# Optimization experiments

Measured on AMD Instinct MI355X. Metric: run time of the kernel, lower is better.

Reference implementation:

```python
import jax, jax.numpy as jnp
import numpy as np

B, F, Hh, Ww, C = 1, 8, 12, 18, 1920
HEADS, HD, RANK, TXT = 30, 64, 128, 224
VID = F * Hh * Ww  # 1728
DN = ('NCH', 'OIH', 'NCH')


def setup_inputs() -> dict:
    key = jax.random.key(0)
    ks = jax.random.split(key, 14)
    s = 0.02
    return {
        'hidden_states': jax.random.normal(ks[0], (B, VID, C), jnp.float32),
        'encoder_hidden_states': jax.random.normal(ks[1], (B, TXT, C), jnp.float32),
        'cos': jax.random.uniform(ks[2], (VID, HD), jnp.float32),
        'sin': jax.random.uniform(ks[3], (VID, HD), jnp.float32),
        'conv1_w': jax.random.normal(ks[4], (RANK, C, 3), jnp.float32) * s,
        'conv2_w': jax.random.normal(ks[5], (C, RANK, 3), jnp.float32) * s,
        'Wq': jax.random.normal(ks[6], (C, C), jnp.float32) * s,
        'bq': jnp.zeros((C,), jnp.float32),
        'Wk': jax.random.normal(ks[7], (C, C), jnp.float32) * s,
        'bk': jnp.zeros((C,), jnp.float32),
        'Wv': jax.random.normal(ks[8], (C, C), jnp.float32) * s,
        'bv': jnp.zeros((C,), jnp.float32),
        'Wo': jax.random.normal(ks[9], (C, C), jnp.float32) * s,
        'bo': jnp.zeros((C,), jnp.float32),
    }


def _rope(x, cos, sin):
    # x: [B, H, S_vid, D]; cos/sin: [S_vid, D]; interleaved rotate-half
    xr = x.reshape(*x.shape[:-1], -1, 2)
    x_rot = jnp.stack([-xr[..., 1], xr[..., 0]], axis=-1).reshape(x.shape)
    return x * cos + x_rot * sin


def reference(hidden_states, encoder_hidden_states, cos, sin, conv1_w, conv2_w,
              Wq, bq, Wk, bk, Wv, bv, Wo, bo):
    # temporal conv1d skip branch over frame axis per spatial location
    x = hidden_states.reshape(B, F, Hh, Ww, C).transpose(0, 2, 3, 4, 1)
    x = x.reshape(B * Hh * Ww, C, F)
    h = jax.lax.conv_general_dilated(x, conv1_w, (1,), [(1, 1)], dimension_numbers=DN)
    h = jax.nn.gelu(h, approximate=False)
    h = jax.lax.conv_general_dilated(h, conv2_w, (1,), [(1, 1)], dimension_numbers=DN)
    skip = h.reshape(B, Hh, Ww, C, F).transpose(0, 4, 1, 2, 3).reshape(B, VID, C)

    hs = jnp.concatenate([encoder_hidden_states, hidden_states + skip], axis=1)  # [B,S,C]

    q = (hs @ Wq.T + bq).reshape(B, -1, HEADS, HD).transpose(0, 2, 1, 3)
    k = (hs @ Wk.T + bk).reshape(B, -1, HEADS, HD).transpose(0, 2, 1, 3)
    v = (hs @ Wv.T + bv).reshape(B, -1, HEADS, HD).transpose(0, 2, 1, 3)

    # RoPE applied only to the video (image) tokens of q and k
    q = jnp.concatenate([q[:, :, :TXT], _rope(q[:, :, TXT:], cos, sin)], axis=2)
    k = jnp.concatenate([k[:, :, :TXT], _rope(k[:, :, TXT:], cos, sin)], axis=2)

    scores = jnp.einsum('bhqd,bhkd->bhqk', q, k) * (HD ** -0.5)
    attn = jax.nn.softmax(scores, axis=-1)
    o = jnp.einsum('bhqk,bhkd->bhqd', attn, v)
    o = o.transpose(0, 2, 1, 3).reshape(B, -1, HEADS * HD)
    o = o @ Wo.T + bo  # to_out[0]; to_out[1] is dropout (identity at eval)

    return (o[:, TXT:], o[:, :TXT])  # (hidden_states, encoder_hidden_states)
```

## Files before the change

kernel.cpp:

```cpp
#include <hip/hip_runtime.h>
#include <math.h>

typedef unsigned short u16;
typedef short short8 __attribute__((ext_vector_type(8)));
typedef short shortv4 __attribute__((ext_vector_type(4)));
typedef float f32x4 __attribute__((ext_vector_type(4)));

#define TXT 224
#define VID 1728
#define S_ALL 1952
#define C_DIM 1920
#define HD 64
#define RANK 128
#define SHD 124928

#define OFF_HS   ((size_t)0)
#define OFF_XPAD ((size_t)3932160)
#define OFF_O    OFF_XPAD
#define OFF_HG   ((size_t)8355840)
#define OFF_W1T  ((size_t)8650752)
#define OFF_W2T  ((size_t)9388032)
#define OFF_WQ   ((size_t)10125312)
#define OFF_WK   ((size_t)13811712)
#define OFF_WV   ((size_t)17498112)
#define OFF_WO   ((size_t)21184512)
#define OFF_Q    ((size_t)24870912)
#define OFF_K    ((size_t)28618752)
#define OFF_V    ((size_t)32366592)

__device__ __forceinline__ float b2f(u16 u) {
  union { unsigned int i; float f; } x; x.i = ((unsigned int)u) << 16; return x.f;
}
__device__ __forceinline__ u16 f2b(float f) {
  union { float f; unsigned int i; } x; x.f = f;
  unsigned int i = x.i;
  return (u16)((i + 0x7FFFu + ((i >> 16) & 1u)) >> 16);
}
__device__ __forceinline__ void gload16(const u16* g, short* l) {
  __builtin_amdgcn_global_load_lds((const __attribute__((address_space(1))) unsigned int*)g,
                                   (__attribute__((address_space(3))) unsigned int*)l, 16, 0, 0);
}

__global__ void __launch_bounds__(256) prep_kernel(const float* __restrict__ hidden,
                                                   const float* __restrict__ enc,
                                                   const float* __restrict__ w1,
                                                   const float* __restrict__ w2,
                                                   const float* __restrict__ Wq,
                                                   const float* __restrict__ Wk,
                                                   const float* __restrict__ Wv,
                                                   const float* __restrict__ Wo,
                                                   u16* __restrict__ ws) {
  size_t i = (size_t)blockIdx.x * 256 + threadIdx.x;
  if (i < 1105920) {
    const size_t e = i * 4;
    const int row = (int)(e / 1920), col = (int)(e % 1920);
    shortv4 o4 = {0, 0, 0, 0};
    if (row >= 216 && row < 1944) {
      const float4 f = *(const float4*)(hidden + (size_t)(row - 216) * 1920 + col);
      o4 = (shortv4){(short)f2b(f.x), (short)f2b(f.y), (short)f2b(f.z), (short)f2b(f.w)};
    }
    *(shortv4*)(ws + OFF_XPAD + e) = o4;
    return;
  }
  i -= 1105920;
  if (i < 184320) {
    const size_t e = i * 4;
    const int r = (int)(e / 5760), j = (int)(e % 5760), t = j / 1920, c = j % 1920;
    const float* s = w1 + (size_t)r * 5760 + (size_t)c * 3 + t;
    shortv4 o4 = {(short)f2b(s[0]), (short)f2b(s[3]), (short)f2b(s[6]), (short)f2b(s[9])};
    *(shortv4*)(ws + OFF_W1T + e) = o4;
    return;
  }
  i -= 184320;
  if (i < 184320) {
    const size_t e = i * 4;
    const int c = (int)(e / 384), j = (int)(e % 384), t = j / 128, r = j % 128;
    const float* s = w2 + (size_t)c * 384 + (size_t)r * 3 + t;
    shortv4 o4 = {(short)f2b(s[0]), (short)f2b(s[3]), (short)f2b(s[6]), (short)f2b(s[9])};
    *(shortv4*)(ws + OFF_W2T + e) = o4;
    return;
  }
  i -= 184320;
  if (i < 107520) {
    const size_t e = i * 4;
    const float4 f = *(const float4*)(enc + e);
    *(shortv4*)(ws + OFF_HS + e) =
        (shortv4){(short)f2b(f.x), (short)f2b(f.y), (short)f2b(f.z), (short)f2b(f.w)};
    return;
  }
  i -= 107520;
  if (i < 3686400) {
    const int j = (int)(i / 921600);
    const size_t e = (i - (size_t)j * 921600) * 4;
    const float* src = (j == 0) ? Wq : ((j == 1) ? Wk : ((j == 2) ? Wv : Wo));
    const float4 f = *(const float4*)(src + e);
    *(shortv4*)(ws + OFF_WQ + (size_t)j * 3686400 + e) =
        (shortv4){(short)f2b(f.x), (short)f2b(f.y), (short)f2b(f.z), (short)f2b(f.w)};
    return;
  }
  i -= 3686400;
  const short8 z8 = {0, 0, 0, 0, 0, 0, 0, 0};
  size_t e;
  if (i < 23040) e = OFF_HS + 3747840 + i * 8;
  else if (i < 26496) e = OFF_HG + (i - 23040) * 8;
  else if (i < 32256) e = OFF_HG + 248832 + (i - 26496) * 8;
  else e = OFF_O + 3747840 + (i - 32256) * 8;
  *(short8*)(ws + e) = z8;
}

struct GArgs {
  const u16 *A, *B0, *B1, *B2;
  const float *bias0, *bias1, *bias2;
  const float *cosp, *sinp, *hidden;
  u16 *out0, *out1, *out2;
  float* outf;
  int lda, ldb, ksteps, spt, tap_rows, nMt, nNt, Mvalid;
};

template <int BM, int BN, int EPI>
__global__ void __launch_bounds__(256) gemm_bt(GArgs a) {
  constexpr int WM = BM / 2, WN = BN / 2, FM = WM / 16, FN = WN / 16;
  __shared__ __align__(16) short lA[BM * 32];
  __shared__ __align__(16) short lB[BN * 32];
  const int tid = threadIdx.x;
  const int lane = tid & 63;
  const int wv = tid >> 6, wr = wv >> 1, wc = wv & 1;
  const int lr = lane & 15, lg = lane >> 4;
  const int mtile = blockIdx.x % a.nMt;
  const int ntile_raw = blockIdx.x / a.nMt;
  const int ntile = ntile_raw % a.nNt;
  const int slice = ntile_raw / a.nNt;
  const int kstart = slice * a.ksteps;
  const int sec = (ntile * BN) / C_DIM;
  const u16* Bw = (sec == 0) ? a.B0 : ((sec == 1) ? a.B1 : a.B2);
  const int nb = ntile * BN - sec * C_DIM;
  const int m0 = mtile * BM;

  f32x4 acc[FM][FN];
#pragma unroll
  for (int i = 0; i < FM; ++i)
#pragma unroll
    for (int j = 0; j < FN; ++j) acc[i][j] = (f32x4){0.f, 0.f, 0.f, 0.f};

  for (int s = 0; s < a.ksteps; ++s) {
    const int gs = kstart + s;
    const int tap = gs / a.spt;
    const int kcol = (gs - tap * a.spt) * 32;
    const int arow0 = m0 + tap * a.tap_rows;
#pragma unroll
    for (int i = 0; i < BM / 64; ++i) {
      const int o = (i * 256 + tid) * 16;
      const int row = o >> 6;
      const int ke = (o & 63) >> 1;
      gload16(a.A + (size_t)(arow0 + row) * a.lda + (kcol + ke), lA + (o >> 1));
    }
#pragma unroll
    for (int i = 0; i < BN / 64; ++i) {
      const int o = (i * 256 + tid) * 16;
      const int row = o >> 6;
      const int ke = (o & 63) >> 1;
      gload16(Bw + (size_t)(nb + row) * a.ldb + (gs * 32 + ke), lB + (o >> 1));
    }
    __syncthreads();
    short8 af[FM], bfr[FN];
#pragma unroll
    for (int i = 0; i < FM; ++i)
      af[i] = *(const short8*)(lA + (wr * WM + i * 16 + lr) * 32 + lg * 8);
#pragma unroll
    for (int j = 0; j < FN; ++j)
      bfr[j] = *(const short8*)(lB + (wc * WN + j * 16 + lr) * 32 + lg * 8);
#pragma unroll
    for (int i = 0; i < FM; ++i)
#pragma unroll
      for (int j = 0; j < FN; ++j)
        acc[i][j] = __builtin_amdgcn_mfma_f32_16x16x32_bf16(af[i], bfr[j], acc[i][j], 0, 0, 0);
    __syncthreads();
  }

#pragma unroll
  for (int i = 0; i < FM; ++i) {
#pragma unroll
    for (int j = 0; j < FN; ++j) {
      const int col = ntile * BN + wc * WN + j * 16 + lr;
#pragma unroll
      for (int r = 0; r < 4; ++r) {
        const int m = m0 + wr * WM + i * 16 + lg * 4 + r;
        float v = acc[i][j][r];
        if (EPI == 4) {
          if (m < a.Mvalid) a.outf[(size_t)slice * 221184 + (size_t)m * RANK + col] = v;
        } else if (EPI == 1) {
          if (m < a.Mvalid) {
            v += a.hidden[(size_t)m * C_DIM + col];
            a.out0[(size_t)m * C_DIM + col] = f2b(v);
          }
        } else if (EPI == 2) {
          const int nn = col - sec * C_DIM;
          const int hh = nn >> 6, d = nn & 63;
          const float* bias = (sec == 0) ? a.bias0 : ((sec == 1) ? a.bias1 : a.bias2);
          v += bias[nn];
          const float vp = __shfl_xor(v, 1);
          if (sec < 2 && m >= TXT) {
            const int vid = ((m < S_ALL) ? m : TXT) - TXT;
            const float c = a.cosp[vid * HD + d];
            const float sn = a.sinp[vid * HD + d];
            v = (d & 1) ? (v * c + vp * sn) : (v * c - vp * sn);
          }
          if (sec == 0) v *= 0.18033688011112042f;
          if (m < a.Mvalid) {
            u16* dst = (sec == 0) ? a.out0 : ((sec == 1) ? a.out1 : a.out2);
            dst[(size_t)hh * SHD + (size_t)m * HD + d] = f2b(v);
          }
        } else {
          v += a.bias0[col];
          if (m < a.Mvalid) {
            const int dr = (m >= TXT) ? (m - TXT) : (VID + m);
            a.outf[(size_t)dr * C_DIM + col] = v;
          }
        }
      }
    }
  }
}

__global__ void __launch_bounds__(256) c1reduce_kernel(const float* __restrict__ part,
                                                       u16* __restrict__ hg) {
  const int i = blockIdx.x * 256 + threadIdx.x;
  float s = 0.f;
#pragma unroll
  for (int j = 0; j < 6; ++j) s += part[(size_t)j * 221184 + i];
  const float g = 0.5f * s * (1.0f + erff(s * 0.70710678f));
  hg[i] = f2b(g);
}

__global__ void __launch_bounds__(256) vtrans_kernel(const u16* __restrict__ vin,
                                                     u16* __restrict__ vout) {
  __shared__ u16 t[64][72];
  const int b = blockIdx.x, hh = b / 31, mt = b % 31;
  const int m0 = mt * 64;
  const int rows = (m0 + 64 <= S_ALL) ? 64 : (S_ALL - m0);
  const int tid = threadIdx.x;
  const u16* src = vin + (size_t)hh * SHD + (size_t)m0 * HD;
#pragma unroll
  for (int p = 0; p < 2; ++p) {
    const int r = p * 32 + (tid >> 3), c = (tid & 7) * 8;
    short8 v8 = {0, 0, 0, 0, 0, 0, 0, 0};
    if (r < rows) v8 = *(const short8*)(src + (size_t)r * HD + c);
    *(short8*)&t[r][c] = v8;
  }
  __syncthreads();
  const int d = tid & 63, ms = tid >> 6;
  if (ms * 16 < rows) {
    short8 a0, a1;
#pragma unroll
    for (int x = 0; x < 8; ++x) { a0[x] = (short)t[ms * 16 + x][d]; a1[x] = (short)t[ms * 16 + 8 + x][d]; }
    u16* dst = vout + (size_t)hh * SHD + (size_t)d * S_ALL + m0 + ms * 16;
    *(short8*)dst = a0;
    *(short8*)(dst + 8) = a1;
  }
}

__global__ void __launch_bounds__(256) attn_kernel(const u16* __restrict__ q,
                                                   const u16* __restrict__ k,
                                                   const u16* __restrict__ vT,
                                                   u16* __restrict__ o) {
  __shared__ __align__(16) short lK[2][4096];
  __shared__ __align__(16) short lV[2][4096];
  __shared__ __align__(16) short lp[4][1024];
  const int bid = blockIdx.x;
  const int hh = bid / 31, qt = bid - hh * 31;
  const int tid = threadIdx.x, wv = tid >> 6, lane = tid & 63;
  const int lr = lane & 15, lg = lane >> 4;
  const int qbase = qt * 64 + wv * 16;
  const bool active = qbase < S_ALL;
  const u16* qh = q + (size_t)hh * SHD;
  const u16* kh = k + (size_t)hh * SHD;
  const u16* vh = vT + (size_t)hh * SHD;

  int krow[2], kcol[2], kdst[2];
#pragma unroll
  for (int j = 0; j < 2; ++j) {
    const int p0 = (j * 256 + tid) * 8;
    const int row = p0 >> 6, cs = p0 & 63;
    kdst[j] = p0;
    krow[j] = row;
    kcol[j] = cs ^ ((row & 7) * 8);
  }

  short8 aq0 = {}, aq1 = {};
  if (active) {
    aq0 = *(const short8*)(qh + (size_t)(qbase + lr) * HD + lg * 8);
    aq1 = *(const short8*)(qh + (size_t)(qbase + lr) * HD + 32 + lg * 8);
  }
  f32x4 oa[4];
#pragma unroll
  for (int gd = 0; gd < 4; ++gd) oa[gd] = (f32x4){0.f, 0.f, 0.f, 0.f};
  float mr = -3.0e38f, lw = 0.f;
  const f32x4 z4 = (f32x4){0.f, 0.f, 0.f, 0.f};
  const int pmask = (lr & 7) * 8;
  short* lpw = &lp[wv][0];

#pragma unroll
  for (int j = 0; j < 2; ++j) gload16(kh + (size_t)krow[j] * HD + kcol[j], &lK[0][kdst[j]]);
#pragma unroll
  for (int j = 0; j < 2; ++j) gload16(vh + (size_t)krow[j] * S_ALL + kcol[j], &lV[0][kdst[j]]);
  __syncthreads();

  int cur = 0;
  for (int t = 0; t < 30; ++t) {
    if (t < 29) {
      const int kb = (t + 1) * 64;
#pragma unroll
      for (int j = 0; j < 2; ++j)
        gload16(kh + (size_t)(kb + krow[j]) * HD + kcol[j], &lK[cur ^ 1][kdst[j]]);
#pragma unroll
      for (int j = 0; j < 2; ++j)
        gload16(vh + (size_t)krow[j] * S_ALL + (kb + kcol[j]), &lV[cur ^ 1][kdst[j]]);
    }
    if (active) {
      const short* Kt = &lK[cur][0];
      const short* Vt = &lV[cur][0];
      f32x4 st[4];
      __builtin_amdgcn_s_setprio(1);
#pragma unroll
      for (int k16 = 0; k16 < 4; ++k16) {
        const int row = k16 * 16 + lr;
        const int m8 = (row & 7) * 8;
        short8 kf0 = *(const short8*)(Kt + row * 64 + ((lg * 8) ^ m8));
        short8 kf1 = *(const short8*)(Kt + row * 64 + ((32 + lg * 8) ^ m8));
        st[k16] = __builtin_amdgcn_mfma_f32_16x16x32_bf16(kf0, aq0, z4, 0, 0, 0);
        st[k16] = __builtin_amdgcn_mfma_f32_16x16x32_bf16(kf1, aq1, st[k16], 0, 0, 0);
      }
      __builtin_amdgcn_s_setprio(0);
      float tm = fmaxf(fmaxf(fmaxf(st[0][0], st[0][1]), fmaxf(st[0][2], st[0][3])),
                       fmaxf(fmaxf(st[1][0], st[1][1]), fmaxf(st[1][2], st[1][3])));
      tm = fmaxf(tm, fmaxf(fmaxf(fmaxf(st[2][0], st[2][1]), fmaxf(st[2][2], st[2][3])),
                           fmaxf(fmaxf(st[3][0], st[3][1]), fmaxf(st[3][2], st[3][3]))));
      tm = fmaxf(tm, __shfl_xor(tm, 16));
      tm = fmaxf(tm, __shfl_xor(tm, 32));
      const bool defer = (__all(tm <= mr + 8.0f) != 0);
      float al = 1.0f;
      if (!defer) {
        const float mn = fmaxf(mr, tm);
        al = __builtin_exp2f(mr - mn);
        mr = mn;
      }
      float rs = 0.f;
#pragma unroll
      for (int k16 = 0; k16 < 4; ++k16) {
        float p0 = __builtin_exp2f(st[k16][0] - mr);
        float p1 = __builtin_exp2f(st[k16][1] - mr);
        float p2 = __builtin_exp2f(st[k16][2] - mr);
        float p3 = __builtin_exp2f(st[k16][3] - mr);
        rs += (p0 + p1) + (p2 + p3);
        uint2 pk;
        asm("v_cvt_pk_bf16_f32 %0, %1, %2" : "=v"(pk.x) : "v"(p0), "v"(p1));
        asm("v_cvt_pk_bf16_f32 %0, %1, %2" : "=v"(pk.y) : "v"(p2), "v"(p3));
        *(uint2*)(lpw + lr * 64 + ((k16 * 16 + lg * 4) ^ pmask)) = pk;
      }
      rs += __shfl_xor(rs, 16);
      rs += __shfl_xor(rs, 32);
      lw = lw * al + rs;
      asm volatile("s_waitcnt lgkmcnt(0)" ::: "memory");
      short8 pa0 = *(const short8*)(lpw + lr * 64 + ((lg * 8) ^ pmask));
      short8 pa1 = *(const short8*)(lpw + lr * 64 + ((32 + lg * 8) ^ pmask));
      float alp[4];
      if (!defer) {
#pragma unroll
        for (int r = 0; r < 4; ++r) alp[r] = __shfl(al, lg * 4 + r);
      }
      __builtin_amdgcn_s_setprio(1);
#pragma unroll
      for (int gd = 0; gd < 4; ++gd) {
        const int row = gd * 16 + lr;
        const int m8 = (row & 7) * 8;
        short8 vf0 = *(const short8*)(Vt + row * 64 + ((lg * 8) ^ m8));
        short8 vf1 = *(const short8*)(Vt + row * 64 + ((32 + lg * 8) ^ m8));
        f32x4 tacc = oa[gd];
        if (!defer) {
#pragma unroll
          for (int r = 0; r < 4; ++r) tacc[r] *= alp[r];
        }
        tacc = __builtin_amdgcn_mfma_f32_16x16x32_bf16(pa0, vf0, tacc, 0, 0, 0);
        oa[gd] = __builtin_amdgcn_mfma_f32_16x16x32_bf16(pa1, vf1, tacc, 0, 0, 0);
      }
      __builtin_amdgcn_s_setprio(0);
    }
    __syncthreads();
    cur ^= 1;
  }

  if (active) {
    const u16* kp = kh + (size_t)1920 * HD;
    short8 kf00 = *(const short8*)(kp + (size_t)lr * HD + lg * 8);
    short8 kf01 = *(const short8*)(kp + (size_t)lr * HD + 32 + lg * 8);
    short8 kf10 = *(const short8*)(kp + (size_t)(16 + lr) * HD + lg * 8);
    short8 kf11 = *(const short8*)(kp + (size_t)(16 + lr) * HD + 32 + lg * 8);
    f32x4 st0 = __builtin_amdgcn_mfma_f32_16x16x32_bf16(kf00, aq0, z4, 0, 0, 0);
    st0 = __builtin_amdgcn_mfma_f32_16x16x32_bf16(kf01, aq1, st0, 0, 0, 0);
    f32x4 st1 = __builtin_amdgcn_mfma_f32_16x16x32_bf16(kf10, aq0, z4, 0, 0, 0);
    st1 = __builtin_amdgcn_mfma_f32_16x16x32_bf16(kf11, aq1, st1, 0, 0, 0);
    float tm = fmaxf(fmaxf(fmaxf(st0[0], st0[1]), fmaxf(st0[2], st0[3])),
                     fmaxf(fmaxf(st1[0], st1[1]), fmaxf(st1[2], st1[3])));
    tm = fmaxf(tm, __shfl_xor(tm, 16));
    tm = fmaxf(tm, __shfl_xor(tm, 32));
    const float mn = fmaxf(mr, tm);
    const float al = __builtin_exp2f(mr - mn);
    mr = mn;
    float rs = 0.f;
    float pp[8];
#pragma unroll
    for (int r = 0; r < 4; ++r) { pp[r] = __builtin_exp2f(st0[r] - mn); rs += pp[r]; }
#pragma unroll
    for (int r = 0; r < 4; ++r) { pp[4 + r] = __builtin_exp2f(st1[r] - mn); rs += pp[4 + r]; }
    {
      uint2 pk;
      asm("v_cvt_pk_bf16_f32 %0, %1, %2" : "=v"(pk.x) : "v"(pp[0]), "v"(pp[1]));
      asm("v_cvt_pk_bf16_f32 %0, %1, %2" : "=v"(pk.y) : "v"(pp[2]), "v"(pp[3]));
      *(uint2*)(lpw + lr * 64 + ((lg * 4) ^ pmask)) = pk;
      asm("v_cvt_pk_bf16_f32 %0, %1, %2" : "=v"(pk.x) : "v"(pp[4]), "v"(pp[5]));
      asm("v_cvt_pk_bf16_f32 %0, %1, %2" : "=v"(pk.y) : "v"(pp[6]), "v"(pp[7]));
      *(uint2*)(lpw + lr * 64 + ((16 + lg * 4) ^ pmask)) = pk;
    }
    rs += __shfl_xor(rs, 16);
    rs += __shfl_xor(rs, 32);
    lw = lw * al + rs;
    asm volatile("s_waitcnt lgkmcnt(0)" ::: "memory");
    short8 pa0 = *(const short8*)(lpw + lr * 64 + ((lg * 8) ^ pmask));
    float alp[4];
#pragma unroll
    for (int r = 0; r < 4; ++r) alp[r] = __shfl(al, lg * 4 + r);
#pragma unroll
    for (int gd = 0; gd < 4; ++gd) {
      short8 vf = *(const short8*)(vh + (size_t)(gd * 16 + lr) * S_ALL + 1920 + lg * 8);
      f32x4 tacc = oa[gd];
#pragma unroll
      for (int r = 0; r < 4; ++r) tacc[r] *= alp[r];
      oa[gd] = __builtin_amdgcn_mfma_f32_16x16x32_bf16(pa0, vf, tacc, 0, 0, 0);
    }
    float lwp[4];
#pragma unroll
    for (int r = 0; r < 4; ++r) lwp[r] = 1.0f / __shfl(lw, lg * 4 + r);
#pragma unroll
    for (int gd = 0; gd < 4; ++gd) {
      const int col = hh * HD + gd * 16 + lr;
#pragma unroll
      for (int r = 0; r < 4; ++r) {
        const int m = qbase + lg * 4 + r;
        o[(size_t)m * C_DIM + col] = f2b(oa[gd][r] * lwp[r]);
      }
    }
  }
}

extern "C" void kernel_launch(void* const* d_in, const int* in_sizes, int n_in,
                              void* d_out, int out_size, void* d_ws, size_t ws_size,
                              hipStream_t stream) {
  const float* hidden = (const float*)d_in[0];
  const float* enc = (const float*)d_in[1];
  const float* cosp = (const float*)d_in[2];
  const float* sinp = (const float*)d_in[3];
  const float* w1 = (const float*)d_in[4];
  const float* w2 = (const float*)d_in[5];
  const float* bq = (const float*)d_in[7];
  const float* bk = (const float*)d_in[9];
  const float* bv = (const float*)d_in[11];
  const float* bo = (const float*)d_in[13];
  u16* ws = (u16*)d_ws;
  float* out = (float*)d_out;

  prep_kernel<<<20796, 256, 0, stream>>>(hidden, enc, w1, w2, (const float*)d_in[6],
                                         (const float*)d_in[8], (const float*)d_in[10],
                                         (const float*)d_in[12], ws);

  GArgs c1{};
  c1.A = ws + OFF_XPAD; c1.B0 = c1.B1 = c1.B2 = ws + OFF_W1T;
  c1.lda = C_DIM; c1.ldb = 5760; c1.ksteps = 30; c1.spt = 60; c1.tap_rows = 216;
  c1.nMt = 27; c1.nNt = 2; c1.Mvalid = VID;
  c1.outf = (float*)(ws + OFF_Q);
  gemm_bt<64, 64, 4><<<324, 256, 0, stream>>>(c1);

  c1reduce_kernel<<<864, 256, 0, stream>>>((const float*)(ws + OFF_Q),
                                           ws + OFF_HG + (size_t)216 * RANK);

  GArgs c2{};
  c2.A = ws + OFF_HG; c2.B0 = c2.B1 = c2.B2 = ws + OFF_W2T;
  c2.lda = RANK; c2.ldb = 384; c2.ksteps = 12; c2.spt = 4; c2.tap_rows = 216;
  c2.nMt = 14; c2.nNt = 15; c2.Mvalid = VID; c2.hidden = hidden;
  c2.out0 = ws + OFF_HS + (size_t)TXT * C_DIM;
  gemm_bt<128, 128, 1><<<210, 256, 0, stream>>>(c2);

  GArgs c3{};
  c3.A = ws + OFF_HS; c3.B0 = ws + OFF_WQ; c3.B1 = ws + OFF_WK; c3.B2 = ws + OFF_WV;
  c3.bias0 = bq; c3.bias1 = bk; c3.bias2 = bv; c3.cosp = cosp; c3.sinp = sinp;
  c3.lda = C_DIM; c3.ldb = C_DIM; c3.ksteps = 60; c3.spt = 60; c3.tap_rows = 0;
  c3.nMt = 16; c3.nNt = 45; c3.Mvalid = S_ALL;
  c3.out0 = ws + OFF_Q; c3.out1 = ws + OFF_K; c3.out2 = ws + OFF_O;
  gemm_bt<128, 128, 2><<<720, 256, 0, stream>>>(c3);

  vtrans_kernel<<<930, 256, 0, stream>>>(ws + OFF_O, ws + OFF_V);

  attn_kernel<<<930, 256, 0, stream>>>(ws + OFF_Q, ws + OFF_K, ws + OFF_V, ws + OFF_O);

  GArgs c4{};
  c4.A = ws + OFF_O; c4.B0 = c4.B1 = c4.B2 = ws + OFF_WO; c4.bias0 = bo;
  c4.lda = C_DIM; c4.ldb = C_DIM; c4.ksteps = 60; c4.spt = 60; c4.tap_rows = 0;
  c4.nMt = 32; c4.nNt = 15; c4.Mvalid = S_ALL;
  c4.outf = out;
  gemm_bt<64, 128, 3><<<480, 256, 0, stream>>>(c4);
}
```

Measured before the change: 273.2 us.

## Double-buffer GEMM LDS tiles and load attention K/V directly from global

```diff
diff --git a/kernel.cpp b/kernel.cpp
--- a/kernel.cpp
+++ b/kernel.cpp
@@ -120,8 +120,8 @@
 template <int BM, int BN, int EPI>
 __global__ void __launch_bounds__(256) gemm_bt(GArgs a) {
   constexpr int WM = BM / 2, WN = BN / 2, FM = WM / 16, FN = WN / 16;
-  __shared__ __align__(16) short lA[BM * 32];
-  __shared__ __align__(16) short lB[BN * 32];
+  __shared__ __align__(16) short lA[2][BM * 32];
+  __shared__ __align__(16) short lB[2][BN * 32];
   const int tid = threadIdx.x;
   const int lane = tid & 63;
   const int wv = tid >> 6, wr = wv >> 1, wc = wv & 1;
@@ -142,8 +142,7 @@
 #pragma unroll
     for (int j = 0; j < FN; ++j) acc[i][j] = (f32x4){0.f, 0.f, 0.f, 0.f};
 
-  for (int s = 0; s < a.ksteps; ++s) {
-    const int gs = kstart + s;
+  auto stageStep = [&](int buf, int gs) {
     const int tap = gs / a.spt;
     const int kcol = (gs - tap * a.spt) * 32;
     const int arow0 = m0 + tap * a.tap_rows;
@@ -152,29 +151,36 @@
       const int o = (i * 256 + tid) * 16;
       const int row = o >> 6;
       const int ke = (o & 63) >> 1;
-      gload16(a.A + (size_t)(arow0 + row) * a.lda + (kcol + ke), lA + (o >> 1));
+      gload16(a.A + (size_t)(arow0 + row) * a.lda + (kcol + ke), &lA[buf][o >> 1]);
     }
 #pragma unroll
     for (int i = 0; i < BN / 64; ++i) {
       const int o = (i * 256 + tid) * 16;
       const int row = o >> 6;
       const int ke = (o & 63) >> 1;
-      gload16(Bw + (size_t)(nb + row) * a.ldb + (gs * 32 + ke), lB + (o >> 1));
-    }
-    __syncthreads();
+      gload16(Bw + (size_t)(nb + row) * a.ldb + (gs * 32 + ke), &lB[buf][o >> 1]);
+    }
+  };
+
+  stageStep(0, kstart);
+  __syncthreads();
+  int cur = 0;
+  for (int s = 0; s < a.ksteps; ++s) {
+    if (s + 1 < a.ksteps) stageStep(cur ^ 1, kstart + s + 1);
     short8 af[FM], bfr[FN];
 #pragma unroll
     for (int i = 0; i < FM; ++i)
-      af[i] = *(const short8*)(lA + (wr * WM + i * 16 + lr) * 32 + lg * 8);
+      af[i] = *(const short8*)(&lA[cur][(wr * WM + i * 16 + lr) * 32 + lg * 8]);
 #pragma unroll
     for (int j = 0; j < FN; ++j)
-      bfr[j] = *(const short8*)(lB + (wc * WN + j * 16 + lr) * 32 + lg * 8);
+      bfr[j] = *(const short8*)(&lB[cur][(wc * WN + j * 16 + lr) * 32 + lg * 8]);
 #pragma unroll
     for (int i = 0; i < FM; ++i)
 #pragma unroll
       for (int j = 0; j < FN; ++j)
         acc[i][j] = __builtin_amdgcn_mfma_f32_16x16x32_bf16(af[i], bfr[j], acc[i][j], 0, 0, 0);
     __syncthreads();
+    cur ^= 1;
   }
 
 #pragma unroll
@@ -263,34 +269,19 @@
                                                    const u16* __restrict__ k,
                                                    const u16* __restrict__ vT,
                                                    u16* __restrict__ o) {
-  __shared__ __align__(16) short lK[2][4096];
-  __shared__ __align__(16) short lV[2][4096];
   __shared__ __align__(16) short lp[4][1024];
   const int bid = blockIdx.x;
   const int hh = bid / 31, qt = bid - hh * 31;
   const int tid = threadIdx.x, wv = tid >> 6, lane = tid & 63;
   const int lr = lane & 15, lg = lane >> 4;
   const int qbase = qt * 64 + wv * 16;
-  const bool active = qbase < S_ALL;
+  if (qbase >= S_ALL) return;
   const u16* qh = q + (size_t)hh * SHD;
   const u16* kh = k + (size_t)hh * SHD;
   const u16* vh = vT + (size_t)hh * SHD;
 
-  int krow[2], kcol[2], kdst[2];
-#pragma unroll
-  for (int j = 0; j < 2; ++j) {
-    const int p0 = (j * 256 + tid) * 8;
-    const int row = p0 >> 6, cs = p0 & 63;
-    kdst[j] = p0;
-    krow[j] = row;
-    kcol[j] = cs ^ ((row & 7) * 8);
-  }
-
-  short8 aq0 = {}, aq1 = {};
-  if (active) {
-    aq0 = *(const short8*)(qh + (size_t)(qbase + lr) * HD + lg * 8);
-    aq1 = *(const short8*)(qh + (size_t)(qbase + lr) * HD + 32 + lg * 8);
-  }
+  short8 aq0 = *(const short8*)(qh + (size_t)(qbase + lr) * HD + lg * 8);
+  short8 aq1 = *(const short8*)(qh + (size_t)(qbase + lr) * HD + 32 + lg * 8);
   f32x4 oa[4];
 #pragma unroll
   for (int gd = 0; gd < 4; ++gd) oa[gd] = (f32x4){0.f, 0.f, 0.f, 0.f};
@@ -298,103 +289,87 @@
   const f32x4 z4 = (f32x4){0.f, 0.f, 0.f, 0.f};
   const int pmask = (lr & 7) * 8;
   short* lpw = &lp[wv][0];
-
-#pragma unroll
-  for (int j = 0; j < 2; ++j) gload16(kh + (size_t)krow[j] * HD + kcol[j], &lK[0][kdst[j]]);
-#pragma unroll
-  for (int j = 0; j < 2; ++j) gload16(vh + (size_t)krow[j] * S_ALL + kcol[j], &lV[0][kdst[j]]);
-  __syncthreads();
-
-  int cur = 0;
+  const u16* krow = kh + (size_t)lr * HD + lg * 8;
+  const u16* vrow[4];
+#pragma unroll
+  for (int gd = 0; gd < 4; ++gd) vrow[gd] = vh + (size_t)(gd * 16 + lr) * S_ALL + lg * 8;
+
   for (int t = 0; t < 30; ++t) {
-    if (t < 29) {
-      const int kb = (t + 1) * 64;
-#pragma unroll
-      for (int j = 0; j < 2; ++j)
-        gload16(kh + (size_t)(kb + krow[j]) * HD + kcol[j], &lK[cur ^ 1][kdst[j]]);
-#pragma unroll
-      for (int j = 0; j < 2; ++j)
-        gload16(vh + (size_t)krow[j] * S_ALL + (kb + kcol[j]), &lV[cur ^ 1][kdst[j]]);
-    }
-    if (active) {
-      const short* Kt = &lK[cur][0];
-      const short* Vt = &lV[cur][0];
-      f32x4 st[4];
-      __builtin_amdgcn_s_setprio(1);
-#pragma unroll
-      for (int k16 = 0; k16 < 4; ++k16) {
-        const int row = k16 * 16 + lr;
-        const int m8 = (row & 7) * 8;
-        short8 kf0 = *(const short8*)(Kt + row * 64 + ((lg * 8) ^ m8));
-        short8 kf1 = *(const short8*)(Kt + row * 64 + ((32 + lg * 8) ^ m8));
-        st[k16] = __builtin_amdgcn_mfma_f32_16x16x32_bf16(kf0, aq0, z4, 0, 0, 0);
-        st[k16] = __builtin_amdgcn_mfma_f32_16x16x32_bf16(kf1, aq1, st[k16], 0, 0, 0);
+    const int kb = t * 64;
+    short8 kf[4][2];
+#pragma unroll
+    for (int k16 = 0; k16 < 4; ++k16) {
+      const u16* kp = krow + (size_t)(kb + k16 * 16) * HD;
+      kf[k16][0] = *(const short8*)(kp);
+      kf[k16][1] = *(const short8*)(kp + 32);
+    }
+    f32x4 st[4];
+    __builtin_amdgcn_s_setprio(1);
+#pragma unroll
+    for (int k16 = 0; k16 < 4; ++k16) {
+      st[k16] = __builtin_amdgcn_mfma_f32_16x16x32_bf16(kf[k16][0], aq0, z4, 0, 0, 0);
+      st[k16] = __builtin_amdgcn_mfma_f32_16x16x32_bf16(kf[k16][1], aq1, st[k16], 0, 0, 0);
+    }
+    __builtin_amdgcn_s_setprio(0);
+    float tm = fmaxf(fmaxf(fmaxf(st[0][0], st[0][1]), fmaxf(st[0][2], st[0][3])),
+                     fmaxf(fmaxf(st[1][0], st[1][1]), fmaxf(st[1][2], st[1][3])));
+    tm = fmaxf(tm, fmaxf(fmaxf(fmaxf(st[2][0], st[2][1]), fmaxf(st[2][2], st[2][3])),
+                         fmaxf(fmaxf(st[3][0], st[3][1]), fmaxf(st[3][2], st[3][3]))));
+    tm = fmaxf(tm, __shfl_xor(tm, 16));
+    tm = fmaxf(tm, __shfl_xor(tm, 32));
+    const bool defer = (__all(tm <= mr + 8.0f) != 0);
+    float al = 1.0f;
+    if (!defer) {
+      const float mn = fmaxf(mr, tm);
+      al = __builtin_exp2f(mr - mn);
+      mr = mn;
+    }
+    float rs = 0.f;
+#pragma unroll
+    for (int k16 = 0; k16 < 4; ++k16) {
+      float p0 = __builtin_exp2f(st[k16][0] - mr);
+      float p1 = __builtin_exp2f(st[k16][1] - mr);
+      float p2 = __builtin_exp2f(st[k16][2] - mr);
+      float p3 = __builtin_exp2f(st[k16][3] - mr);
+      rs += (p0 + p1) + (p2 + p3);
+      uint2 pk;
+      asm("v_cvt_pk_bf16_f32 %0, %1, %2" : "=v"(pk.x) : "v"(p0), "v"(p1));
+      asm("v_cvt_pk_bf16_f32 %0, %1, %2" : "=v"(pk.y) : "v"(p2), "v"(p3));
+      *(uint2*)(lpw + lr * 64 + ((k16 * 16 + lg * 4) ^ pmask)) = pk;
+    }
+    rs += __shfl_xor(rs, 16);
+    rs += __shfl_xor(rs, 32);
+    lw = lw * al + rs;
+    asm volatile("s_waitcnt lgkmcnt(0)" ::: "memory");
+    short8 pa0 = *(const short8*)(lpw + lr * 64 + ((lg * 8) ^ pmask));
+    short8 pa1 = *(const short8*)(lpw + lr * 64 + ((32 + lg * 8) ^ pmask));
+    float alp[4];
+    if (!defer) {
+#pragma unroll
+      for (int r = 0; r < 4; ++r) alp[r] = __shfl(al, lg * 4 + r);
+    }
+    __builtin_amdgcn_s_setprio(1);
+#pragma unroll
+    for (int gd = 0; gd < 4; ++gd) {
+      short8 vf0 = *(const short8*)(vrow[gd] + kb);
+      short8 vf1 = *(const short8*)(vrow[gd] + kb + 32);
+      f32x4 tacc = oa[gd];
+      if (!defer) {
+#pragma unroll
+        for (int r = 0; r < 4; ++r) tacc[r] *= alp[r];
       }
-      __builtin_amdgcn_s_setprio(0);
-      float tm = fmaxf(fmaxf(fmaxf(st[0][0], st[0][1]), fmaxf(st[0][2], st[0][3])),
-                       fmaxf(fmaxf(st[1][0], st[1][1]), fmaxf(st[1][2], st[1][3])));
-      tm = fmaxf(tm, fmaxf(fmaxf(fmaxf(st[2][0], st[2][1]), fmaxf(st[2][2], st[2][3])),
-                           fmaxf(fmaxf(st[3][0], st[3][1]), fmaxf(st[3][2], st[3][3]))));
-      tm = fmaxf(tm, __shfl_xor(tm, 16));
-      tm = fmaxf(tm, __shfl_xor(tm, 32));
-      const bool defer = (__all(tm <= mr + 8.0f) != 0);
-      float al = 1.0f;
-      if (!defer) {
-        const float mn = fmaxf(mr, tm);
-        al = __builtin_exp2f(mr - mn);
-        mr = mn;
-      }
-      float rs = 0.f;
-#pragma unroll
-      for (int k16 = 0; k16 < 4; ++k16) {
-        float p0 = __builtin_exp2f(st[k16][0] - mr);
-        float p1 = __builtin_exp2f(st[k16][1] - mr);
-        float p2 = __builtin_exp2f(st[k16][2] - mr);
-        float p3 = __builtin_exp2f(st[k16][3] - mr);
-        rs += (p0 + p1) + (p2 + p3);
-        uint2 pk;
-        asm("v_cvt_pk_bf16_f32 %0, %1, %2" : "=v"(pk.x) : "v"(p0), "v"(p1));
-        asm("v_cvt_pk_bf16_f32 %0, %1, %2" : "=v"(pk.y) : "v"(p2), "v"(p3));
-        *(uint2*)(lpw + lr * 64 + ((k16 * 16 + lg * 4) ^ pmask)) = pk;
-      }
-      rs += __shfl_xor(rs, 16);
-      rs += __shfl_xor(rs, 32);
-      lw = lw * al + rs;
-      asm volatile("s_waitcnt lgkmcnt(0)" ::: "memory");
-      short8 pa0 = *(const short8*)(lpw + lr * 64 + ((lg * 8) ^ pmask));
-      short8 pa1 = *(const short8*)(lpw + lr * 64 + ((32 + lg * 8) ^ pmask));
-      float alp[4];
-      if (!defer) {
-#pragma unroll
-        for (int r = 0; r < 4; ++r) alp[r] = __shfl(al, lg * 4 + r);
-      }
-      __builtin_amdgcn_s_setprio(1);
-#pragma unroll
-      for (int gd = 0; gd < 4; ++gd) {
-        const int row = gd * 16 + lr;
-        const int m8 = (row & 7) * 8;
-        short8 vf0 = *(const short8*)(Vt + row * 64 + ((lg * 8) ^ m8));
-        short8 vf1 = *(const short8*)(Vt + row * 64 + ((32 + lg * 8) ^ m8));
-        f32x4 tacc = oa[gd];
-        if (!defer) {
-#pragma unroll
-          for (int r = 0; r < 4; ++r) tacc[r] *= alp[r];
-        }
-        tacc = __builtin_amdgcn_mfma_f32_16x16x32_bf16(pa0, vf0, tacc, 0, 0, 0);
-        oa[gd] = __builtin_amdgcn_mfma_f32_16x16x32_bf16(pa1, vf1, tacc, 0, 0, 0);
-      }
-      __builtin_amdgcn_s_setprio(0);
-    }
-    __syncthreads();
-    cur ^= 1;
-  }
-
-  if (active) {
-    const u16* kp = kh + (size_t)1920 * HD;
-    short8 kf00 = *(const short8*)(kp + (size_t)lr * HD + lg * 8);
-    short8 kf01 = *(const short8*)(kp + (size_t)lr * HD + 32 + lg * 8);
-    short8 kf10 = *(const short8*)(kp + (size_t)(16 + lr) * HD + lg * 8);
-    short8 kf11 = *(const short8*)(kp + (size_t)(16 + lr) * HD + 32 + lg * 8);
+      tacc = __builtin_amdgcn_mfma_f32_16x16x32_bf16(pa0, vf0, tacc, 0, 0, 0);
+      oa[gd] = __builtin_amdgcn_mfma_f32_16x16x32_bf16(pa1, vf1, tacc, 0, 0, 0);
+    }
+    __builtin_amdgcn_s_setprio(0);
+  }
+
+  {
+    const u16* kp = krow + (size_t)1920 * HD;
+    short8 kf00 = *(const short8*)(kp);
+    short8 kf01 = *(const short8*)(kp + 32);
+    short8 kf10 = *(const short8*)(kp + 16 * HD);
+    short8 kf11 = *(const short8*)(kp + 16 * HD + 32);
     f32x4 st0 = __builtin_amdgcn_mfma_f32_16x16x32_bf16(kf00, aq0, z4, 0, 0, 0);
     st0 = __builtin_amdgcn_mfma_f32_16x16x32_bf16(kf01, aq1, st0, 0, 0, 0);
     f32x4 st1 = __builtin_amdgcn_mfma_f32_16x16x32_bf16(kf10, aq0, z4, 0, 0, 0);
@@ -431,7 +406,7 @@
     for (int r = 0; r < 4; ++r) alp[r] = __shfl(al, lg * 4 + r);
 #pragma unroll
     for (int gd = 0; gd < 4; ++gd) {
-      short8 vf = *(const short8*)(vh + (size_t)(gd * 16 + lr) * S_ALL + 1920 + lg * 8);
+      short8 vf = *(const short8*)(vrow[gd] + 1920);
       f32x4 tacc = oa[gd];
 #pragma unroll
       for (int r = 0; r < 4; ++r) tacc[r] *= alp[r];
```

After: 347.9 us. +27.4%, slower.

## Double-buffer GEMM LDS tiles and load attention V fragments directly from global

Applied to the files above, without the earlier changes.

```diff
diff --git a/kernel.cpp b/kernel.cpp
--- a/kernel.cpp
+++ b/kernel.cpp
@@ -120,8 +120,8 @@
 template <int BM, int BN, int EPI>
 __global__ void __launch_bounds__(256) gemm_bt(GArgs a) {
   constexpr int WM = BM / 2, WN = BN / 2, FM = WM / 16, FN = WN / 16;
-  __shared__ __align__(16) short lA[BM * 32];
-  __shared__ __align__(16) short lB[BN * 32];
+  __shared__ __align__(16) short lA[2][BM * 32];
+  __shared__ __align__(16) short lB[2][BN * 32];
   const int tid = threadIdx.x;
   const int lane = tid & 63;
   const int wv = tid >> 6, wr = wv >> 1, wc = wv & 1;
@@ -142,8 +142,7 @@
 #pragma unroll
     for (int j = 0; j < FN; ++j) acc[i][j] = (f32x4){0.f, 0.f, 0.f, 0.f};
 
-  for (int s = 0; s < a.ksteps; ++s) {
-    const int gs = kstart + s;
+  auto stageStep = [&](int buf, int gs) {
     const int tap = gs / a.spt;
     const int kcol = (gs - tap * a.spt) * 32;
     const int arow0 = m0 + tap * a.tap_rows;
@@ -152,29 +151,36 @@
       const int o = (i * 256 + tid) * 16;
       const int row = o >> 6;
       const int ke = (o & 63) >> 1;
-      gload16(a.A + (size_t)(arow0 + row) * a.lda + (kcol + ke), lA + (o >> 1));
+      gload16(a.A + (size_t)(arow0 + row) * a.lda + (kcol + ke), &lA[buf][o >> 1]);
     }
 #pragma unroll
     for (int i = 0; i < BN / 64; ++i) {
       const int o = (i * 256 + tid) * 16;
       const int row = o >> 6;
       const int ke = (o & 63) >> 1;
-      gload16(Bw + (size_t)(nb + row) * a.ldb + (gs * 32 + ke), lB + (o >> 1));
-    }
-    __syncthreads();
+      gload16(Bw + (size_t)(nb + row) * a.ldb + (gs * 32 + ke), &lB[buf][o >> 1]);
+    }
+  };
+
+  stageStep(0, kstart);
+  __syncthreads();
+  int cur = 0;
+  for (int s = 0; s < a.ksteps; ++s) {
+    if (s + 1 < a.ksteps) stageStep(cur ^ 1, kstart + s + 1);
     short8 af[FM], bfr[FN];
 #pragma unroll
     for (int i = 0; i < FM; ++i)
-      af[i] = *(const short8*)(lA + (wr * WM + i * 16 + lr) * 32 + lg * 8);
+      af[i] = *(const short8*)(&lA[cur][(wr * WM + i * 16 + lr) * 32 + lg * 8]);
 #pragma unroll
     for (int j = 0; j < FN; ++j)
-      bfr[j] = *(const short8*)(lB + (wc * WN + j * 16 + lr) * 32 + lg * 8);
+      bfr[j] = *(const short8*)(&lB[cur][(wc * WN + j * 16 + lr) * 32 + lg * 8]);
 #pragma unroll
     for (int i = 0; i < FM; ++i)
 #pragma unroll
       for (int j = 0; j < FN; ++j)
         acc[i][j] = __builtin_amdgcn_mfma_f32_16x16x32_bf16(af[i], bfr[j], acc[i][j], 0, 0, 0);
     __syncthreads();
+    cur ^= 1;
   }
 
 #pragma unroll
@@ -264,7 +270,6 @@
                                                    const u16* __restrict__ vT,
                                                    u16* __restrict__ o) {
   __shared__ __align__(16) short lK[2][4096];
-  __shared__ __align__(16) short lV[2][4096];
   __shared__ __align__(16) short lp[4][1024];
   const int bid = blockIdx.x;
   const int hh = bid / 31, qt = bid - hh * 31;
@@ -298,27 +303,24 @@
   const f32x4 z4 = (f32x4){0.f, 0.f, 0.f, 0.f};
   const int pmask = (lr & 7) * 8;
   short* lpw = &lp[wv][0];
+  const u16* vrow[4];
+#pragma unroll
+  for (int gd = 0; gd < 4; ++gd) vrow[gd] = vh + (size_t)(gd * 16 + lr) * S_ALL + lg * 8;
 
 #pragma unroll
   for (int j = 0; j < 2; ++j) gload16(kh + (size_t)krow[j] * HD + kcol[j], &lK[0][kdst[j]]);
-#pragma unroll
-  for (int j = 0; j < 2; ++j) gload16(vh + (size_t)krow[j] * S_ALL + kcol[j], &lV[0][kdst[j]]);
   __syncthreads();
 
   int cur = 0;
   for (int t = 0; t < 30; ++t) {
+    const int kb = t * 64;
     if (t < 29) {
-      const int kb = (t + 1) * 64;
 #pragma unroll
       for (int j = 0; j < 2; ++j)
-        gload16(kh + (size_t)(kb + krow[j]) * HD + kcol[j], &lK[cur ^ 1][kdst[j]]);
-#pragma unroll
-      for (int j = 0; j < 2; ++j)
-        gload16(vh + (size_t)krow[j] * S_ALL + (kb + kcol[j]), &lV[cur ^ 1][kdst[j]]);
+        gload16(kh + (size_t)(kb + 64 + krow[j]) * HD + kcol[j], &lK[cur ^ 1][kdst[j]]);
     }
     if (active) {
       const short* Kt = &lK[cur][0];
-      const short* Vt = &lV[cur][0];
       f32x4 st[4];
       __builtin_amdgcn_s_setprio(1);
 #pragma unroll
@@ -331,6 +333,12 @@
         st[k16] = __builtin_amdgcn_mfma_f32_16x16x32_bf16(kf1, aq1, st[k16], 0, 0, 0);
       }
       __builtin_amdgcn_s_setprio(0);
+      short8 vf[4][2];
+#pragma unroll
+      for (int gd = 0; gd < 4; ++gd) {
+        vf[gd][0] = *(const short8*)(vrow[gd] + kb);
+        vf[gd][1] = *(const short8*)(vrow[gd] + kb + 32);
+      }
       float tm = fmaxf(fmaxf(fmaxf(st[0][0], st[0][1]), fmaxf(st[0][2], st[0][3])),
                        fmaxf(fmaxf(st[1][0], st[1][1]), fmaxf(st[1][2], st[1][3])));
       tm = fmaxf(tm, fmaxf(fmaxf(fmaxf(st[2][0], st[2][1]), fmaxf(st[2][2], st[2][3])),
@@ -371,17 +379,13 @@
       __builtin_amdgcn_s_setprio(1);
 #pragma unroll
       for (int gd = 0; gd < 4; ++gd) {
-        const int row = gd * 16 + lr;
-        const int m8 = (row & 7) * 8;
-        short8 vf0 = *(const short8*)(Vt + row * 64 + ((lg * 8) ^ m8));
-        short8 vf1 = *(const short8*)(Vt + row * 64 + ((32 + lg * 8) ^ m8));
         f32x4 tacc = oa[gd];
         if (!defer) {
 #pragma unroll
           for (int r = 0; r < 4; ++r) tacc[r] *= alp[r];
         }
-        tacc = __builtin_amdgcn_mfma_f32_16x16x32_bf16(pa0, vf0, tacc, 0, 0, 0);
-        oa[gd] = __builtin_amdgcn_mfma_f32_16x16x32_bf16(pa1, vf1, tacc, 0, 0, 0);
+        tacc = __builtin_amdgcn_mfma_f32_16x16x32_bf16(pa0, vf[gd][0], tacc, 0, 0, 0);
+        oa[gd] = __builtin_amdgcn_mfma_f32_16x16x32_bf16(pa1, vf[gd][1], tacc, 0, 0, 0);
       }
       __builtin_amdgcn_s_setprio(0);
     }
@@ -390,11 +394,11 @@
   }
 
   if (active) {
-    const u16* kp = kh + (size_t)1920 * HD;
-    short8 kf00 = *(const short8*)(kp + (size_t)lr * HD + lg * 8);
-    short8 kf01 = *(const short8*)(kp + (size_t)lr * HD + 32 + lg * 8);
-    short8 kf10 = *(const short8*)(kp + (size_t)(16 + lr) * HD + lg * 8);
-    short8 kf11 = *(const short8*)(kp + (size_t)(16 + lr) * HD + 32 + lg * 8);
+    const u16* kp = kh + (size_t)1920 * HD + (size_t)lr * HD + lg * 8;
+    short8 kf00 = *(const short8*)(kp);
+    short8 kf01 = *(const short8*)(kp + 32);
+    short8 kf10 = *(const short8*)(kp + 16 * HD);
+    short8 kf11 = *(const short8*)(kp + 16 * HD + 32);
     f32x4 st0 = __builtin_amdgcn_mfma_f32_16x16x32_bf16(kf00, aq0, z4, 0, 0, 0);
     st0 = __builtin_amdgcn_mfma_f32_16x16x32_bf16(kf01, aq1, st0, 0, 0, 0);
     f32x4 st1 = __builtin_amdgcn_mfma_f32_16x16x32_bf16(kf10, aq0, z4, 0, 0, 0);
@@ -431,7 +435,7 @@
     for (int r = 0; r < 4; ++r) alp[r] = __shfl(al, lg * 4 + r);
 #pragma unroll
     for (int gd = 0; gd < 4; ++gd) {
-      short8 vf = *(const short8*)(vh + (size_t)(gd * 16 + lr) * S_ALL + 1920 + lg * 8);
+      short8 vf = *(const short8*)(vrow[gd] + 1920);
       f32x4 tacc = oa[gd];
 #pragma unroll
       for (int r = 0; r < 4; ++r) tacc[r] *= alp[r];
```

New measurement: 299.2 us. 9.5% more time.
